# Kernel optimization log

Measured on AMD Instinct MI355X. Metric: run time of the kernel, lower is better.

Reference implementation:

```python
import jax, jax.numpy as jnp
import numpy as np

TOP_K = 4
MAX_NUM_BINS = 32
HIDDEN = 64
STAT_DIM = 4 * (TOP_K + 1)  # 20


def setup_inputs() -> dict:
    key = jax.random.key(0)
    k1, k2, k3, k4 = jax.random.split(key, 4)
    B, L, C = 16, 32768, 80
    scores = jax.random.normal(k1, (B, L, C), dtype=jnp.float32)
    pred_corners = jax.random.normal(k2, (B, L, 4 * (MAX_NUM_BINS + 1)), dtype=jnp.float32)
    # reg_conf MLP params: Dense(20->64) relu, Dense(64->1)
    W1 = jax.random.normal(k3, (STAT_DIM, HIDDEN), dtype=jnp.float32) * (1.0 / np.sqrt(STAT_DIM))
    b1 = jnp.zeros((HIDDEN,), dtype=jnp.float32)
    W2 = jax.random.normal(k4, (HIDDEN, 1), dtype=jnp.float32) * (1.0 / np.sqrt(HIDDEN))
    b2 = jnp.zeros((1,), dtype=jnp.float32)
    return {"scores": scores, "pred_corners": pred_corners,
            "W1": W1, "b1": b1, "W2": W2, "b2": b2}


def reference(scores, pred_corners, W1, b1, W2, b2):
    B, L, _ = pred_corners.shape
    # (B, L, 4, bins+1)
    corners = pred_corners.reshape(B, L, 4, MAX_NUM_BINS + 1)
    prob = jax.nn.softmax(corners, axis=-1)
    # sorted (descending) top-k over bin dim -> (B, L, 4, TOP_K)
    prob_topk, _ = jax.lax.top_k(prob, TOP_K)
    # concat mean -> (B, L, 4, TOP_K+1), then flatten -> (B, L, 20)
    stat = jnp.concatenate(
        [prob_topk, jnp.mean(prob_topk, axis=-1, keepdims=True)], axis=-1)
    stat = stat.reshape(B, L, STAT_DIM)
    # tiny 2-layer MLP -> quality score (B, L, 1)
    h = jax.nn.relu(jnp.einsum("bld,dh->blh", stat, W1) + b1)
    quality = jnp.einsum("blh,ho->blo", h, W2) + b2
    return scores + quality
```

## Files before the change

### kernel.cpp

```cpp
#include <hip/hip_runtime.h>
#include <math.h>

#define TOPK   4
#define NBINS  33
#define SIDES  4
#define CPA    132
#define STATD  20
#define HID    64
#define NCLS   80
#define APB    64
#define BS     256

__global__ __launch_bounds__(BS) void lqe_kernel(
    const float* __restrict__ scores,
    const float* __restrict__ corners,
    const float* __restrict__ W1,
    const float* __restrict__ b1,
    const float* __restrict__ W2,
    const float* __restrict__ b2,
    float* __restrict__ out)
{
    __shared__ float s_corners[APB * CPA];
    __shared__ float s_stat[APB * STATD];
    __shared__ float s_q[APB];
    __shared__ float s_W1[STATD * HID];
    __shared__ float s_b1[HID];
    __shared__ float s_W2[HID];
    __shared__ float s_b2;

    const int tid = threadIdx.x;
    const long long aBase = (long long)blockIdx.x * APB;

    for (int i = tid; i < STATD * HID; i += BS) s_W1[i] = W1[i];
    if (tid < HID) { s_b1[tid] = b1[tid]; s_W2[tid] = W2[tid]; }
    if (tid == 0)  { s_b2 = b2[0]; }

    {
        const float4* src = (const float4*)(corners + aBase * CPA);
        float4* dst = (float4*)s_corners;
        #pragma unroll
        for (int i = tid; i < (APB * CPA) / 4; i += BS) dst[i] = src[i];
    }
    __syncthreads();

    {
        const int a    = tid >> 2;
        const int side = tid & 3;
        const float* pc = s_corners + a * CPA + side * NBINS;

        float p[NBINS];
        #pragma unroll
        for (int k = 0; k < NBINS; ++k) p[k] = pc[k];

        float m = p[0];
        #pragma unroll
        for (int k = 1; k < NBINS; ++k) m = fmaxf(m, p[k]);

        float s = 0.0f;
        #pragma unroll
        for (int k = 0; k < NBINS; ++k) { p[k] = __expf(p[k] - m); s += p[k]; }

        float top[TOPK];
        #pragma unroll
        for (int j = 0; j < TOPK; ++j) {
            float best = -1.0f; int bi = 0;
            #pragma unroll
            for (int k = 0; k < NBINS; ++k) {
                if (p[k] > best) { best = p[k]; bi = k; }
            }
            top[j] = best;
            #pragma unroll
            for (int k = 0; k < NBINS; ++k) p[k] = (k == bi) ? -1.0f : p[k];
        }

        const float inv = 1.0f / s;
        const float t0 = top[0] * inv, t1 = top[1] * inv;
        const float t2 = top[2] * inv, t3 = top[3] * inv;
        const float mean = (t0 + t1 + t2 + t3) * 0.25f;

        float* st = s_stat + a * STATD + side * (TOPK + 1);
        st[0] = t0; st[1] = t1; st[2] = t2; st[3] = t3; st[4] = mean;
    }
    __syncthreads();

    {
        const int wave = tid >> 6;
        const int lane = tid & 63;
        #pragma unroll
        for (int i = 0; i < APB / 4; ++i) {
            const int a = wave * (APB / 4) + i;
            float acc = s_b1[lane];
            #pragma unroll
            for (int d = 0; d < STATD; ++d)
                acc = fmaf(s_stat[a * STATD + d], s_W1[d * HID + lane], acc);
            float hv = fmaxf(acc, 0.0f) * s_W2[lane];
            #pragma unroll
            for (int mk = 32; mk >= 1; mk >>= 1)
                hv += __shfl_xor(hv, mk, 64);
            if (lane == 0) s_q[a] = hv + s_b2;
        }
    }
    __syncthreads();

    {
        const float4* sc = (const float4*)(scores + aBase * NCLS);
        float4* op = (float4*)(out + aBase * NCLS);
        #pragma unroll
        for (int j = tid; j < (APB * NCLS) / 4; j += BS) {
            const float q = s_q[j / (NCLS / 4)];
            float4 v = sc[j];
            v.x += q; v.y += q; v.z += q; v.w += q;
            op[j] = v;
        }
    }
}

extern "C" void kernel_launch(void* const* d_in, const int* in_sizes, int n_in,
                              void* d_out, int out_size, void* d_ws, size_t ws_size,
                              hipStream_t stream) {
    const float* scores  = (const float*)d_in[0];
    const float* corners = (const float*)d_in[1];
    const float* W1      = (const float*)d_in[2];
    const float* b1      = (const float*)d_in[3];
    const float* W2      = (const float*)d_in[4];
    const float* b2      = (const float*)d_in[5];
    float* out = (float*)d_out;

    const int nAnchors = in_sizes[0] / NCLS;
    const int blocks = nAnchors / APB;
    lqe_kernel<<<blocks, BS, 0, stream>>>(scores, corners, W1, b1, W2, b2, out);
}
```

Before: 594.0 us.

## Split into quality and add kernels, register-cache W1, use insertion top-k

Splits the fused kernel into two launches: one computes per-anchor quality into a workspace buffer, and the other adds it to the scores. The W1 column, bias and W2 now live in registers instead of shared memory. Top-k uses a single-pass min/max insertion network instead of four argmax passes, and the stat rows are read as float4. This cuts shared memory and ALU work so more blocks fit per CU, in exchange for an extra launch and a small round-trip of q through global memory.

```diff
diff --git a/kernel.cpp b/kernel.cpp
--- a/kernel.cpp
+++ b/kernel.cpp
@@ -3,7 +3,6 @@
 
 #define TOPK   4
 #define NBINS  33
-#define SIDES  4
 #define CPA    132
 #define STATD  20
 #define HID    64
@@ -11,29 +10,26 @@
 #define APB    64
 #define BS     256
 
-__global__ __launch_bounds__(BS) void lqe_kernel(
-    const float* __restrict__ scores,
+__global__ __launch_bounds__(BS, 4) void lqe_quality(
     const float* __restrict__ corners,
     const float* __restrict__ W1,
     const float* __restrict__ b1,
     const float* __restrict__ W2,
     const float* __restrict__ b2,
-    float* __restrict__ out)
+    float* __restrict__ q)
 {
     __shared__ float s_corners[APB * CPA];
     __shared__ float s_stat[APB * STATD];
-    __shared__ float s_q[APB];
-    __shared__ float s_W1[STATD * HID];
-    __shared__ float s_b1[HID];
-    __shared__ float s_W2[HID];
-    __shared__ float s_b2;
 
-    const int tid = threadIdx.x;
+    const int tid  = threadIdx.x;
+    const int lane = tid & 63;
     const long long aBase = (long long)blockIdx.x * APB;
 
-    for (int i = tid; i < STATD * HID; i += BS) s_W1[i] = W1[i];
-    if (tid < HID) { s_b1[tid] = b1[tid]; s_W2[tid] = W2[tid]; }
-    if (tid == 0)  { s_b2 = b2[0]; }
+    float w1c[STATD];
+    #pragma unroll
+    for (int d = 0; d < STATD; ++d) w1c[d] = W1[d * HID + lane];
+    const float bias = b1[lane];
+    const float w2v  = W2[lane];
 
     {
         const float4* src = (const float4*)(corners + aBase * CPA);
@@ -60,22 +56,19 @@
         #pragma unroll
         for (int k = 0; k < NBINS; ++k) { p[k] = __expf(p[k] - m); s += p[k]; }
 
-        float top[TOPK];
+        float t0 = -1.0f, t1 = -1.0f, t2 = -1.0f, t3 = -1.0f;
         #pragma unroll
-        for (int j = 0; j < TOPK; ++j) {
-            float best = -1.0f; int bi = 0;
-            #pragma unroll
-            for (int k = 0; k < NBINS; ++k) {
-                if (p[k] > best) { best = p[k]; bi = k; }
-            }
-            top[j] = best;
-            #pragma unroll
-            for (int k = 0; k < NBINS; ++k) p[k] = (k == bi) ? -1.0f : p[k];
+        for (int k = 0; k < NBINS; ++k) {
+            const float v  = p[k];
+            const float b0 = fmaxf(t0, v),  c0 = fminf(t0, v);
+            const float b1_ = fmaxf(t1, c0), c1 = fminf(t1, c0);
+            const float b2_ = fmaxf(t2, c1), c2 = fminf(t2, c1);
+            const float b3 = fmaxf(t3, c2);
+            t0 = b0; t1 = b1_; t2 = b2_; t3 = b3;
         }
 
         const float inv = 1.0f / s;
-        const float t0 = top[0] * inv, t1 = top[1] * inv;
-        const float t2 = top[2] * inv, t3 = top[3] * inv;
+        t0 *= inv; t1 *= inv; t2 *= inv; t3 *= inv;
         const float mean = (t0 + t1 + t2 + t3) * 0.25f;
 
         float* st = s_stat + a * STATD + side * (TOPK + 1);
@@ -85,33 +78,52 @@
 
     {
         const int wave = tid >> 6;
-        const int lane = tid & 63;
+        const float b2v = b2[0];
         #pragma unroll
         for (int i = 0; i < APB / 4; ++i) {
             const int a = wave * (APB / 4) + i;
-            float acc = s_b1[lane];
-            #pragma unroll
-            for (int d = 0; d < STATD; ++d)
-                acc = fmaf(s_stat[a * STATD + d], s_W1[d * HID + lane], acc);
-            float hv = fmaxf(acc, 0.0f) * s_W2[lane];
+            const float4* sp = (const float4*)(s_stat + a * STATD);
+            const float4 s0 = sp[0], s1 = sp[1], s2 = sp[2], s3 = sp[3], s4 = sp[4];
+            float acc = bias;
+            acc = fmaf(s0.x, w1c[0],  acc); acc = fmaf(s0.y, w1c[1],  acc);
+            acc = fmaf(s0.z, w1c[2],  acc); acc = fmaf(s0.w, w1c[3],  acc);
+            acc = fmaf(s1.x, w1c[4],  acc); acc = fmaf(s1.y, w1c[5],  acc);
+            acc = fmaf(s1.z, w1c[6],  acc); acc = fmaf(s1.w, w1c[7],  acc);
+            acc = fmaf(s2.x, w1c[8],  acc); acc = fmaf(s2.y, w1c[9],  acc);
+            acc = fmaf(s2.z, w1c[10], acc); acc = fmaf(s2.w, w1c[11], acc);
+            acc = fmaf(s3.x, w1c[12], acc); acc = fmaf(s3.y, w1c[13], acc);
+            acc = fmaf(s3.z, w1c[14], acc); acc = fmaf(s3.w, w1c[15], acc);
+            acc = fmaf(s4.x, w1c[16], acc); acc = fmaf(s4.y, w1c[17], acc);
+            acc = fmaf(s4.z, w1c[18], acc); acc = fmaf(s4.w, w1c[19], acc);
+            float hv = fmaxf(acc, 0.0f) * w2v;
             #pragma unroll
             for (int mk = 32; mk >= 1; mk >>= 1)
                 hv += __shfl_xor(hv, mk, 64);
-            if (lane == 0) s_q[a] = hv + s_b2;
+            if (lane == 0) q[aBase + a] = hv + b2v;
         }
     }
+}
+
+__global__ __launch_bounds__(BS) void lqe_add(
+    const float* __restrict__ scores,
+    const float* __restrict__ q,
+    float* __restrict__ out)
+{
+    __shared__ float s_q[APB];
+    const int tid = threadIdx.x;
+    const long long aBase = (long long)blockIdx.x * APB;
+
+    if (tid < APB) s_q[tid] = q[aBase + tid];
     __syncthreads();
 
-    {
-        const float4* sc = (const float4*)(scores + aBase * NCLS);
-        float4* op = (float4*)(out + aBase * NCLS);
-        #pragma unroll
-        for (int j = tid; j < (APB * NCLS) / 4; j += BS) {
-            const float q = s_q[j / (NCLS / 4)];
-            float4 v = sc[j];
-            v.x += q; v.y += q; v.z += q; v.w += q;
-            op[j] = v;
-        }
+    const float4* sc = (const float4*)(scores + aBase * NCLS);
+    float4* op = (float4*)(out + aBase * NCLS);
+    #pragma unroll
+    for (int j = tid; j < (APB * NCLS) / 4; j += BS) {
+        const float qv = s_q[j / (NCLS / 4)];
+        float4 v = sc[j];
+        v.x += qv; v.y += qv; v.z += qv; v.w += qv;
+        op[j] = v;
     }
 }
 
@@ -125,8 +137,11 @@
     const float* W2      = (const float*)d_in[4];
     const float* b2      = (const float*)d_in[5];
     float* out = (float*)d_out;
+    float* q   = (float*)d_ws;
 
     const int nAnchors = in_sizes[0] / NCLS;
-    const int blocks = nAnchors / APB;
-    lqe_kernel<<<blocks, BS, 0, stream>>>(scores, corners, W1, b1, W2, b2, out);
+    const int blocks   = nAnchors / APB;
+
+    lqe_quality<<<blocks, BS, 0, stream>>>(corners, W1, b1, W2, b2, q);
+    lqe_add<<<blocks, BS, 0, stream>>>(scores, q, out);
 }
```

After: 544.9 us. -8.3%, faster.
